# Optimization experiments

Hardware: AMD Instinct MI355X
Metric: run time of the kernel (lower is better)

## Reference

```python
import jax, jax.numpy as jnp
import numpy as np

K = 15  # kNN neighbors, matches init kwarg


def _knn_edges(x, k):
    # brute-force kNN, flow='target_to_source': row = center node, col = neighbor
    sq = jnp.sum(x * x, axis=-1)
    d2 = sq[:, None] - 2.0 * (x @ x.T) + sq[None, :]          # [N,N]
    n = x.shape[0]
    d2 = jnp.where(jnp.eye(n, dtype=bool), jnp.inf, d2)        # exclude self-loops
    _, idx = jax.lax.top_k(-d2, k)                             # [N,k] nearest
    row = jnp.repeat(jnp.arange(n), k)
    col = idx.reshape(-1)
    return jnp.stack([row, col])                               # [2, N*k]


def _scatter_softmax(a, seg, n):
    m = jax.ops.segment_max(a, seg, num_segments=n)
    m = jnp.where(jnp.isfinite(m), m, 0.0)
    e = jnp.exp(a - m[seg])
    s = jax.ops.segment_sum(e, seg, num_segments=n)
    return e / s[seg]


def _devconv(x, edges, W_theta, b_theta, W_phi, b_phi):
    # DevConv (neural mesh simplification): W_phi . max_{j in N(i)} W_theta(x_i - x_j)
    row, col = edges[0], edges[1]
    h = (x[row] - x[col]) @ W_theta.T + b_theta                # [E, H]
    agg = jax.ops.segment_max(h, row, num_segments=x.shape[0])  # [N, H]
    agg = jnp.where(jnp.isfinite(agg), agg, 0.0)               # guard empty rows
    return agg @ W_phi.T + b_phi


def setup_inputs() -> dict:
    key = jax.random.key(0)
    ks = jax.random.split(key, 8)
    N, E, H, C = 4096, 65536, 64, 3
    x = jax.random.normal(ks[0], (N, C), dtype=jnp.float32)
    edge_index = jax.random.randint(ks[1], (2, E), 0, N, dtype=jnp.int64)
    s_in, s_h = 1.0 / np.sqrt(C), 1.0 / np.sqrt(H)
    return {
        "x": x,
        "edge_index": edge_index,
        "W_theta": jax.random.normal(ks[2], (H, C), dtype=jnp.float32) * s_in,
        "b_theta": jnp.zeros((H,), dtype=jnp.float32),
        "W_phi": jax.random.normal(ks[3], (H, H), dtype=jnp.float32) * s_h,
        "b_phi": jnp.zeros((H,), dtype=jnp.float32),
        "W_q": jax.random.normal(ks[4], (H, H), dtype=jnp.float32) * s_h,
        "W_k": jax.random.normal(ks[5], (H, H), dtype=jnp.float32) * s_h,
    }


def reference(x, edge_index, W_theta, b_theta, W_phi, b_phi, W_q, W_k):
    n = x.shape[0]
    knn = _knn_edges(x, K)
    extended = jnp.concatenate([edge_index, knn], axis=1)
    feats = _devconv(x, extended, W_theta, b_theta, W_phi, b_phi)  # [N, H]
    row, col = edge_index[0], edge_index[1]
    q = feats @ W_q.T
    kf = feats @ W_k.T
    attn = jnp.sum(q[row] * kf[col], axis=-1)                  # [E]
    scores = _scatter_softmax(attn, row, n)                     # [E]
    # S, A as dense NxN (duplicates summed, matching sparse coalescing)
    S = jnp.zeros((n, n), dtype=x.dtype).at[row, col].add(scores)
    A = jnp.zeros((n, n), dtype=x.dtype).at[row, col].add(1.0)
    A_s = S @ A @ S.T                                           # simplified adjacency
    return A_s
```

## Files before the change

kernel.cpp:

```cpp
#include <hip/hip_runtime.h>
#include <math.h>

#define HN 64
#define KNN 15
#define MAXT 768

__device__ __forceinline__ unsigned fenc(float f){
  unsigned u = __float_as_uint(f);
  return (u & 0x80000000u) ? ~u : (u | 0x80000000u);
}

__device__ __forceinline__ unsigned long long u64min(unsigned long long a, unsigned long long b){
  return a < b ? a : b;
}
__device__ __forceinline__ unsigned long long shfl_xor_u64(unsigned long long v, int mask){
  unsigned lo = (unsigned)v, hi = (unsigned)(v >> 32);
  lo = __shfl_xor((int)lo, mask, 64);
  hi = __shfl_xor((int)hi, mask, 64);
  return ((unsigned long long)hi << 32) | lo;
}

__device__ __forceinline__ void edge_load(const void* ei, int E, int n, int e, int& r, int& c){
  const long long* L = (const long long*)ei;
  long long vr = L[e];
  bool ok = (vr >= 0 && vr < (long long)n);
  unsigned long long bal = __ballot(ok);
  unsigned long long act = __ballot(true);
  if (bal == act){
    r = (int)vr;
    c = (int)L[E + e];
  } else {
    const int* I = (const int*)ei;
    r = I[e];
    c = I[E + e];
  }
}

__global__ void __launch_bounds__(256) k_mega(
    const float* __restrict__ x, const float* __restrict__ Wt, const void* ei,
    float* __restrict__ y, int* __restrict__ knn_cols,
    int* __restrict__ cnt, int* __restrict__ ccnt,
    int N, int E, int nbY, int nbC){
  __shared__ unsigned denc[4096];
  __shared__ unsigned long long mk[256];
  int b = blockIdx.x, t = threadIdx.x;
  if (b < nbY){
    int gid = b * 256 + t;
    if (gid < N * HN){
      int nn = gid >> 6, h = gid & 63;
      y[gid] = x[nn*3] * Wt[h*3] + x[nn*3+1] * Wt[h*3+1] + x[nn*3+2] * Wt[h*3+2];
    }
    return;
  }
  if (b < nbY + nbC){
    int e = (b - nbY) * 256 + t;
    if (e < E){
      int r, c;
      edge_load(ei, E, N, e, r, c);
      atomicAdd(&cnt[r], 1);
      atomicAdd(&ccnt[c], 1);
    }
    return;
  }
  int i = b - nbY - nbC;
  float xi0 = x[i*3], xi1 = x[i*3+1], xi2 = x[i*3+2];
  float sqi = xi0*xi0 + xi1*xi1 + xi2*xi2;
  unsigned long long best = ~0ULL;
  #pragma unroll
  for (int m = 0; m < 16; ++m){
    int j = t + 256*m;
    float a = x[j*3], bb = x[j*3+1], c = x[j*3+2];
    float sqj = a*a + bb*bb + c*c;
    float dot = xi0*a + xi1*bb + xi2*c;
    float d2 = (sqi - 2.0f*dot) + sqj;
    unsigned e = (j == i) ? 0xFFFFFFFFu : fenc(d2);
    denc[j] = e;
    best = u64min(best, ((unsigned long long)e << 32) | (unsigned)j);
  }
  mk[t] = best;
  __syncthreads();
  if (t >= 64) return;
  unsigned long long k0 = mk[t], k1 = mk[t+64], k2 = mk[t+128], k3 = mk[t+192];
  for (int m = 0; m < KNN; ++m){
    unsigned long long mm = u64min(u64min(k0, k1), u64min(k2, k3));
    #pragma unroll
    for (int off = 1; off < 64; off <<= 1)
      mm = u64min(mm, shfl_xor_u64(mm, off));
    int j = (int)(mm & 0xFFFFFFFFu);
    if (t == 0) knn_cols[i*KNN + m] = j;
    if ((j & 63) == t){
      int slot = j & 255;
      denc[j] = 0xFFFFFFFFu;
      unsigned long long nb = ~0ULL;
      #pragma unroll
      for (int m2 = 0; m2 < 16; ++m2){
        int jj = slot + 256*m2;
        nb = u64min(nb, ((unsigned long long)denc[jj] << 32) | (unsigned)jj);
      }
      int kreg = (j >> 6) & 3;
      if (kreg == 0) k0 = nb; else if (kreg == 1) k1 = nb;
      else if (kreg == 2) k2 = nb; else k3 = nb;
    }
  }
}

__global__ void k_scan2(const int* __restrict__ cnt, int* __restrict__ ptr,
                        const int* __restrict__ ccnt, int* __restrict__ cptr,
                        int2* __restrict__ rinfo, int2* __restrict__ cinfo, int n){
  __shared__ int part[1024];
  const int* src = (blockIdx.x == 0) ? cnt : ccnt;
  int* dst = (blockIdx.x == 0) ? ptr : cptr;
  int t = threadIdx.x;
  int base = t * 4;
  int a0 = src[base], a1 = src[base+1], a2 = src[base+2], a3 = src[base+3];
  int s = a0 + a1 + a2 + a3;
  part[t] = s;
  __syncthreads();
  for (int off = 1; off < 1024; off <<= 1){
    int v = (t >= off) ? part[t - off] : 0;
    __syncthreads();
    part[t] += v;
    __syncthreads();
  }
  int excl = part[t] - s;
  int v0 = excl, v1 = excl + a0, v2 = excl + a0 + a1, v3 = excl + a0 + a1 + a2;
  dst[base]   = v0;
  dst[base+1] = v1;
  dst[base+2] = v2;
  dst[base+3] = v3;
  if (t == 1023) dst[n] = part[1023];
  if (blockIdx.x == 0){
    rinfo[base]   = make_int2(v0 + KNN*base,     a0);
    rinfo[base+1] = make_int2(v1 + KNN*(base+1), a1);
    rinfo[base+2] = make_int2(v2 + KNN*(base+2), a2);
    rinfo[base+3] = make_int2(v3 + KNN*(base+3), a3);
  } else {
    cinfo[base]   = make_int2(v0, a0);
    cinfo[base+1] = make_int2(v1, a1);
    cinfo[base+2] = make_int2(v2, a2);
    cinfo[base+3] = make_int2(v3, a3);
  }
}

__global__ void k_fill(const void* ei, const int* __restrict__ ptr,
                       int* __restrict__ fillo, const int* __restrict__ cnt,
                       const int* __restrict__ knncols, int* __restrict__ ecol,
                       int N, int E, int nbE){
  int b = blockIdx.x, t = threadIdx.x;
  if (b < nbE){
    int e = b * 256 + t;
    if (e < E){
      int r, c;
      edge_load(ei, E, N, e, r, c);
      int pos = ptr[r] + KNN*r + atomicAdd(&fillo[r], 1);
      ecol[pos] = c;
    }
  } else {
    int gid = (b - nbE) * 256 + t;
    if (gid < N * KNN){
      int i = gid / KNN, m = gid - i * KNN;
      ecol[ptr[i] + KNN*i + cnt[i] + m] = knncols[gid];
    }
  }
}

__global__ void k_dev(const int* __restrict__ ptr, const int* __restrict__ ecol,
                      const float* __restrict__ y, const float* __restrict__ bt,
                      const float* __restrict__ Wp, const float* __restrict__ bp,
                      const float* __restrict__ Wq, const float* __restrict__ Wk,
                      float* __restrict__ q, float* __restrict__ kf, int n){
  __shared__ float sag[256];
  __shared__ float sft[256];
  int t = threadIdx.x;
  int i = blockIdx.x * 4 + (t >> 6);
  int h = t & 63;
  int beg = ptr[i] + KNN*i;
  int end = ptr[i+1] + KNN*(i+1);
  float m = INFINITY;
  for (int idx = beg; idx < end; ++idx)
    m = fminf(m, y[ecol[idx]*HN + h]);
  sag[t] = y[i*HN + h] + bt[h] - m;
  __syncthreads();
  int nn = t >> 6;
  float acc = bp[h];
  #pragma unroll 8
  for (int c = 0; c < HN; ++c) acc += sag[nn*HN + c] * Wp[h*HN + c];
  sft[t] = acc;
  __syncthreads();
  float aq = 0.f, ak = 0.f;
  #pragma unroll 8
  for (int c = 0; c < HN; ++c){
    float f = sft[nn*HN + c];
    aq += f * Wq[h*HN + c];
    ak += f * Wk[h*HN + c];
  }
  size_t o = (size_t)blockIdx.x * 256 + t;
  q[o] = aq;
  kf[o] = ak;
}

__global__ void __launch_bounds__(256) k_rowattn(
    const int* __restrict__ ptr, const int2* __restrict__ cinfo,
    const int* __restrict__ ecol, const float* __restrict__ q,
    const float* __restrict__ kf, float* __restrict__ sval,
    int2* __restrict__ scp, int2* __restrict__ csp,
    int* __restrict__ cfill, int n){
  int t = threadIdx.x;
  int lane = t & 63;
  int r = blockIdx.x * 4 + (t >> 6);
  if (r >= n) return;
  int base = ptr[r];
  int deg = ptr[r+1] - base;
  if (deg == 0) return;
  int ebase = base + KNN*r;
  float4 qv[16];
  const float4* qr = (const float4*)(q + (size_t)r*HN);
  #pragma unroll
  for (int m = 0; m < 16; ++m) qv[m] = qr[m];
  float mx = -INFINITY;
  for (int s = lane; s < deg; s += 64){
    int c = ecol[ebase + s];
    const float4* kc = (const float4*)(kf + (size_t)c*HN);
    float acc = 0.f;
    #pragma unroll
    for (int m = 0; m < 16; ++m){
      float4 b = kc[m];
      acc += qv[m].x*b.x + qv[m].y*b.y + qv[m].z*b.z + qv[m].w*b.w;
    }
    sval[base + s] = acc;
    mx = fmaxf(mx, acc);
  }
  #pragma unroll
  for (int off = 1; off < 64; off <<= 1) mx = fmaxf(mx, __shfl_xor(mx, off, 64));
  float lsum = 0.f;
  for (int s = lane; s < deg; s += 64){
    float e = expf(sval[base + s] - mx);
    sval[base + s] = e;
    lsum += e;
  }
  #pragma unroll
  for (int off = 1; off < 64; off <<= 1) lsum += __shfl_xor(lsum, off, 64);
  for (int s = lane; s < deg; s += 64){
    float v = sval[base + s] / lsum;
    int c = ecol[ebase + s];
    scp[base + s] = make_int2(c, __float_as_int(v));
    int2 ci = cinfo[c];
    int pos = ci.x + atomicAdd(&cfill[c], 1);
    csp[pos] = make_int2(r, __float_as_int(v));
  }
}

__global__ void __launch_bounds__(256) k_tbuild(
    const int2* __restrict__ rinfo, const int* __restrict__ ecol,
    const int2* __restrict__ cinfo, const int2* __restrict__ csp,
    int2* __restrict__ tlist, int* __restrict__ tcnt, int n){
  __shared__ float Drow[4096];
  __shared__ int   tag[4096];
  __shared__ int   pre[65];
  __shared__ int   csrc[64];
  __shared__ int   wsum[4];
  int k = blockIdx.x, t = threadIdx.x, lane = t & 63, wid = t >> 6;
  float4* D4 = (float4*)Drow;
  float4 fz = {0.f, 0.f, 0.f, 0.f};
  #pragma unroll
  for (int j = 0; j < 4; ++j) D4[j*256 + t] = fz;
  int2 ri = rinfo[k];
  int nseg = min(ri.y, 64);
  if (t < 64){
    int v = 0, src = 0;
    if (lane < nseg){
      int c = ecol[ri.x + lane];
      int2 ci = cinfo[c];
      v = ci.y; src = ci.x;
    }
    csrc[lane] = src;
    int ps = v;
    #pragma unroll
    for (int off = 1; off < 64; off <<= 1){
      int o = __shfl_up(ps, off, 64);
      if (lane >= off) ps += o;
    }
    pre[lane + 1] = ps;
    if (lane == 0) pre[0] = 0;
  }
  __syncthreads();
  int total = min(pre[nseg], MAXT);
  int er[3]; float ev[3]; bool edone[3];
  #pragma unroll
  for (int j = 0; j < 3; ++j){
    int d = t + 256*j;
    edone[j] = true;
    er[j] = 0; ev[j] = 0.f;
    if (d < total){
      int lo = 0, hi = nseg - 1;
      while (lo < hi){
        int mid = (lo + hi + 1) >> 1;
        if (pre[mid] <= d) lo = mid; else hi = mid - 1;
      }
      int2 e = csp[csrc[lo] + (d - pre[lo])];
      er[j] = e.x; ev[j] = __int_as_float(e.y); edone[j] = false;
    }
  }
  int wr[3]; int wn = 0;
  int round = 0;
  while (true){
    #pragma unroll
    for (int j = 0; j < 3; ++j) if (!edone[j]) tag[er[j]] = t + 256*j;
    __syncthreads();
    bool any = false;
    #pragma unroll
    for (int j = 0; j < 3; ++j) if (!edone[j]){
      if (tag[er[j]] == t + 256*j){
        Drow[er[j]] += ev[j];
        edone[j] = true;
        if (round == 0) wr[wn++] = er[j];
      } else any = true;
    }
    ++round;
    if (__syncthreads_count(any ? 1 : 0) == 0) break;
    if (round >= MAXT) break;
  }
  int v = wn;
  #pragma unroll
  for (int off = 1; off < 64; off <<= 1){
    int o = __shfl_up(v, off, 64);
    if (lane >= off) v += o;
  }
  if (lane == 63) wsum[wid] = v;
  __syncthreads();
  int base0 = 0;
  #pragma unroll
  for (int w = 0; w < 4; ++w) if (w < wid) base0 += wsum[w];
  int excl = base0 + v - wn;
  int2* trow = tlist + (size_t)k * MAXT;
  #pragma unroll
  for (int j = 0; j < 3; ++j) if (j < wn)
    trow[excl + j] = make_int2(wr[j], __float_as_int(Drow[wr[j]]));
  if (t == 0) tcnt[k] = wsum[0] + wsum[1] + wsum[2] + wsum[3];
}

__global__ void __launch_bounds__(64) k_papply(
    const int* __restrict__ ptr, const int2* __restrict__ scp,
    const int2* __restrict__ tlist, const int* __restrict__ tcnt,
    float* __restrict__ out, int n){
  __shared__ float orow[4096];
  int i = blockIdx.x, t = threadIdx.x;
  float4* o4 = (float4*)orow;
  float4 z = {0.f, 0.f, 0.f, 0.f};
  #pragma unroll
  for (int j = 0; j < 16; ++j) o4[j*64 + t] = z;
  int base = ptr[i], len = ptr[i+1] - base;
  for (int p = 0; p < len; ++p){
    int2 kv = scp[base + p];
    int k = kv.x;
    float v = __int_as_float(kv.y);
    int tc = tcnt[k];
    const int2* trow = tlist + (size_t)k * MAXT;
    for (int d = t; d < tc; d += 64){
      int2 e = trow[d];
      orow[e.x] += v * __int_as_float(e.y);
    }
  }
  float4* dst = (float4*)(out + (size_t)i * n);
  #pragma unroll
  for (int j = 0; j < 16; ++j) dst[j*64 + t] = o4[j*64 + t];
}

extern "C" void kernel_launch(void* const* d_in, const int* in_sizes, int n_in,
                              void* d_out, int out_size, void* d_ws, size_t ws_size,
                              hipStream_t stream) {
  const float* x   = (const float*)d_in[0];
  const void*  ei  = d_in[1];
  const float* Wt  = (const float*)d_in[2];
  const float* bt  = (const float*)d_in[3];
  const float* Wp  = (const float*)d_in[4];
  const float* bp  = (const float*)d_in[5];
  const float* Wq  = (const float*)d_in[6];
  const float* Wk  = (const float*)d_in[7];
  float* out = (float*)d_out;

  const int N = in_sizes[0] / 3;
  const int E = in_sizes[1] / 2;

  char* p = (char*)d_ws;
  auto alloc = [&](size_t bytes) -> void* {
    void* r = (void*)p;
    p += (bytes + 255) & ~(size_t)255;
    return r;
  };
  int*      ctr     = (int*)  alloc((size_t)4*N*4);
  int*      cnt     = ctr;
  int*      ccnt    = ctr + N;
  int*      cfill   = ctr + 2*N;
  int*      fillo   = ctr + 3*N;

  float*    y       = (float*)alloc((size_t)N*HN*4);
  float*    q       = (float*)alloc((size_t)N*HN*4);
  float*    kf      = (float*)alloc((size_t)N*HN*4);
  int*      ptrb    = (int*)  alloc((size_t)(N+1)*4);
  int*      cptrb   = (int*)  alloc((size_t)(N+1)*4);
  int2*     rinfo   = (int2*) alloc((size_t)N*8);
  int2*     cinfo   = (int2*) alloc((size_t)N*8);
  int*      ecol    = (int*)  alloc((size_t)(E + N*KNN)*4);
  float*    sval    = (float*)alloc((size_t)E*4);
  int2*     scp     = (int2*) alloc((size_t)E*8);
  int2*     csp     = (int2*) alloc((size_t)E*8);
  int*      knncols = (int*)  alloc((size_t)N*KNN*4);
  int*      tcnt    = (int*)  alloc((size_t)N*4);
  int2*     tlist   = (int2*) alloc((size_t)N*MAXT*8);

  hipMemsetAsync(ctr, 0, (size_t)4*N*4, stream);

  int nbY = (N*HN + 255)/256;
  int nbC = (E + 255)/256;
  int nbK = (N*KNN + 255)/256;

  k_mega<<<nbY + nbC + N, 256, 0, stream>>>(x, Wt, ei, y, knncols, cnt, ccnt,
                                            N, E, nbY, nbC);
  k_scan2<<<2, 1024, 0, stream>>>(cnt, ptrb, ccnt, cptrb, rinfo, cinfo, N);
  k_fill<<<nbC + nbK, 256, 0, stream>>>(ei, ptrb, fillo, cnt, knncols, ecol,
                                        N, E, nbC);
  k_dev<<<N/4, 256, 0, stream>>>(ptrb, ecol, y, bt, Wp, bp, Wq, Wk, q, kf, N);
  k_rowattn<<<N/4, 256, 0, stream>>>(ptrb, cinfo, ecol, q, kf, sval, scp, csp,
                                     cfill, N);
  k_tbuild<<<N, 256, 0, stream>>>(rinfo, ecol, cinfo, csp, tlist, tcnt, N);
  k_papply<<<N, 64, 0, stream>>>(ptrb, scp, tlist, tcnt, out, N);
}
```

Measured before the change: 311.9 us.

## Bucket T rows by column quarter so papply waves own disjoint output ranges

k_tbuild now sorts each sparse row of T into four column-quarter buckets and stores per-quarter counts as an int4. k_papply then uses 512-thread blocks that handle two output rows, with each wave owning one 1024-column quarter. This removes the cross-lane shared-memory read-modify-write conflicts between waves and raises per-block parallelism beyond a single 64-thread wave. The cost is extra counting and scan work in tbuild and possible load imbalance across quarters.

```diff
diff --git a/kernel.cpp b/kernel.cpp
--- a/kernel.cpp
+++ b/kernel.cpp
@@ -253,12 +253,13 @@
 __global__ void __launch_bounds__(256) k_tbuild(
     const int2* __restrict__ rinfo, const int* __restrict__ ecol,
     const int2* __restrict__ cinfo, const int2* __restrict__ csp,
-    int2* __restrict__ tlist, int* __restrict__ tcnt, int n){
+    int2* __restrict__ tlist, int4* __restrict__ tqcnt, int n){
   __shared__ float Drow[4096];
   __shared__ int   tag[4096];
   __shared__ int   pre[65];
   __shared__ int   csrc[64];
-  __shared__ int   wsum[4];
+  __shared__ int   wsumA[4];
+  __shared__ int   wsumB[4];
   int k = blockIdx.x, t = threadIdx.x, lane = t & 63, wid = t >> 6;
   float4* D4 = (float4*)Drow;
   float4 fz = {0.f, 0.f, 0.f, 0.f};
@@ -320,50 +321,84 @@
     if (__syncthreads_count(any ? 1 : 0) == 0) break;
     if (round >= MAXT) break;
   }
-  int v = wn;
+  int n0 = 0, n1 = 0, n2 = 0, n3 = 0;
+  #pragma unroll
+  for (int j = 0; j < 3; ++j) if (j < wn){
+    int qq = wr[j] >> 10;
+    if (qq == 0) ++n0; else if (qq == 1) ++n1; else if (qq == 2) ++n2; else ++n3;
+  }
+  int packA = n0 | (n1 << 16);
+  int packB = n2 | (n3 << 16);
+  int sA = packA, sB = packB;
   #pragma unroll
   for (int off = 1; off < 64; off <<= 1){
-    int o = __shfl_up(v, off, 64);
-    if (lane >= off) v += o;
-  }
-  if (lane == 63) wsum[wid] = v;
-  __syncthreads();
-  int base0 = 0;
-  #pragma unroll
-  for (int w = 0; w < 4; ++w) if (w < wid) base0 += wsum[w];
-  int excl = base0 + v - wn;
+    int oA = __shfl_up(sA, off, 64);
+    int oB = __shfl_up(sB, off, 64);
+    if (lane >= off){ sA += oA; sB += oB; }
+  }
+  if (lane == 63){ wsumA[wid] = sA; wsumB[wid] = sB; }
+  __syncthreads();
+  int baseA = 0, baseB = 0;
+  #pragma unroll
+  for (int w = 0; w < 4; ++w) if (w < wid){ baseA += wsumA[w]; baseB += wsumB[w]; }
+  int exclA = baseA + sA - packA;
+  int exclB = baseB + sB - packB;
+  int totalA = wsumA[0] + wsumA[1] + wsumA[2] + wsumA[3];
+  int totalB = wsumB[0] + wsumB[1] + wsumB[2] + wsumB[3];
+  int T0 = totalA & 0xffff, T1 = totalA >> 16;
+  int T2 = totalB & 0xffff, T3 = totalB >> 16;
+  int pos0 = (exclA & 0xffff);
+  int pos1 = T0 + (exclA >> 16);
+  int pos2 = T0 + T1 + (exclB & 0xffff);
+  int pos3 = T0 + T1 + T2 + (exclB >> 16);
   int2* trow = tlist + (size_t)k * MAXT;
   #pragma unroll
-  for (int j = 0; j < 3; ++j) if (j < wn)
-    trow[excl + j] = make_int2(wr[j], __float_as_int(Drow[wr[j]]));
-  if (t == 0) tcnt[k] = wsum[0] + wsum[1] + wsum[2] + wsum[3];
-}
-
-__global__ void __launch_bounds__(64) k_papply(
+  for (int j = 0; j < 3; ++j) if (j < wn){
+    int r = wr[j];
+    int qq = r >> 10;
+    int pos;
+    if (qq == 0) pos = pos0++; else if (qq == 1) pos = pos1++;
+    else if (qq == 2) pos = pos2++; else pos = pos3++;
+    trow[pos] = make_int2(r, __float_as_int(Drow[r]));
+  }
+  if (t == 0) tqcnt[k] = make_int4(T0, T1, T2, T3);
+}
+
+__global__ void __launch_bounds__(512) k_papply(
     const int* __restrict__ ptr, const int2* __restrict__ scp,
-    const int2* __restrict__ tlist, const int* __restrict__ tcnt,
+    const int2* __restrict__ tlist, const int4* __restrict__ tqcnt,
     float* __restrict__ out, int n){
-  __shared__ float orow[4096];
-  int i = blockIdx.x, t = threadIdx.x;
-  float4* o4 = (float4*)orow;
+  __shared__ float orow[2][4096];
+  int t = threadIdx.x;
+  int half = t >> 8;
+  int wv = (t >> 6) & 3;
+  int lane = t & 63;
+  int i = blockIdx.x * 2 + half;
+  float* my = orow[half];
+  float4* oq = (float4*)(my + wv * 1024);
   float4 z = {0.f, 0.f, 0.f, 0.f};
   #pragma unroll
-  for (int j = 0; j < 16; ++j) o4[j*64 + t] = z;
+  for (int j = 0; j < 4; ++j) oq[j*64 + lane] = z;
   int base = ptr[i], len = ptr[i+1] - base;
   for (int p = 0; p < len; ++p){
     int2 kv = scp[base + p];
     int k = kv.x;
     float v = __int_as_float(kv.y);
-    int tc = tcnt[k];
-    const int2* trow = tlist + (size_t)k * MAXT;
-    for (int d = t; d < tc; d += 64){
+    int4 tq = tqcnt[k];
+    int off, cnt;
+    if (wv == 0){ off = 0;                  cnt = tq.x; }
+    else if (wv == 1){ off = tq.x;          cnt = tq.y; }
+    else if (wv == 2){ off = tq.x + tq.y;   cnt = tq.z; }
+    else { off = tq.x + tq.y + tq.z;        cnt = tq.w; }
+    const int2* trow = tlist + (size_t)k * MAXT + off;
+    for (int d = lane; d < cnt; d += 64){
       int2 e = trow[d];
-      orow[e.x] += v * __int_as_float(e.y);
-    }
-  }
-  float4* dst = (float4*)(out + (size_t)i * n);
-  #pragma unroll
-  for (int j = 0; j < 16; ++j) dst[j*64 + t] = o4[j*64 + t];
+      my[e.x] += v * __int_as_float(e.y);
+    }
+  }
+  float4* dst = (float4*)(out + (size_t)i * n + wv * 1024);
+  #pragma unroll
+  for (int j = 0; j < 4; ++j) dst[j*64 + lane] = oq[j*64 + lane];
 }
 
 extern "C" void kernel_launch(void* const* d_in, const int* in_sizes, int n_in,
@@ -406,7 +441,7 @@
   int2*     scp     = (int2*) alloc((size_t)E*8);
   int2*     csp     = (int2*) alloc((size_t)E*8);
   int*      knncols = (int*)  alloc((size_t)N*KNN*4);
-  int*      tcnt    = (int*)  alloc((size_t)N*4);
+  int4*     tqcnt   = (int4*) alloc((size_t)N*16);
   int2*     tlist   = (int2*) alloc((size_t)N*MAXT*8);
 
   hipMemsetAsync(ctr, 0, (size_t)4*N*4, stream);
@@ -423,6 +458,6 @@
   k_dev<<<N/4, 256, 0, stream>>>(ptrb, ecol, y, bt, Wp, bp, Wq, Wk, q, kf, N);
   k_rowattn<<<N/4, 256, 0, stream>>>(ptrb, cinfo, ecol, q, kf, sval, scp, csp,
                                      cfill, N);
-  k_tbuild<<<N, 256, 0, stream>>>(rinfo, ecol, cinfo, csp, tlist, tcnt, N);
-  k_papply<<<N, 64, 0, stream>>>(ptrb, scp, tlist, tcnt, out, N);
-}
+  k_tbuild<<<N, 256, 0, stream>>>(rinfo, ecol, cinfo, csp, tlist, tqcnt, N);
+  k_papply<<<N/2, 512, 0, stream>>>(ptrb, scp, tlist, tqcnt, out, N);
+}
```

Result: faster. 302.4 us (-3.1%).
